# Optimization experiments

Hardware: AMD Instinct MI355X
Metric: run time of the kernel (lower is better)

Reference implementation:

```python
import jax, jax.numpy as jnp
import numpy as np

B, P, N, E, F, L = 64, 512, 512, 128, 512, 6
SQRT_E = 11.313708498984761
CLIP = 10.0
EPS = 1e-5

def _inorm(x, w, b):
    # InstanceNorm1d over node dim (axis=1) per (batch, channel); x: [B,N,E]
    mu = x.mean(axis=1, keepdims=True)
    var = x.var(axis=1, keepdims=True)
    return (x - mu) * jax.lax.rsqrt(var + EPS) * w + b

def setup_inputs():
    key = jax.random.key(0)
    ks = jax.random.split(key, 24)
    nrm = lambda k, shp, s=0.05: jax.random.normal(k, shp, dtype=jnp.float32) * s
    inp = {}
    inp['data'] = jax.random.uniform(ks[0], (B, N, 2), dtype=jnp.float32)
    inp['dist'] = -jax.random.uniform(ks[1], (B, N, N), dtype=jnp.float32)      # negative dist
    inp['cur_dist'] = -jax.random.uniform(ks[2], (B, P, N), dtype=jnp.float32)
    inp['capacity'] = jax.random.uniform(ks[3], (B, P), dtype=jnp.float32)
    inp['ninf_mask'] = jnp.zeros((B, P, N), jnp.float32)
    inp['log_scale'] = jnp.array([1.0], jnp.float32)
    # encoder params (Linear weights stored [in,out], i.e. torch weight transposed)
    inp['emb_W'] = nrm(ks[4], (2, E), 0.5); inp['emb_b'] = jnp.zeros((E,), jnp.float32)
    inp['Wq'] = nrm(ks[5], (L, E, E)); inp['Wk'] = nrm(ks[6], (L, E, E)); inp['Wv'] = nrm(ks[7], (L, E, E))
    inp['aft_alpha'] = jnp.ones((L,), jnp.float32)
    inp['n1_w'] = jnp.ones((L, E), jnp.float32); inp['n1_b'] = jnp.zeros((L, E), jnp.float32)
    inp['ff_W1'] = nrm(ks[8], (L, E, F)); inp['ff_b1'] = jnp.zeros((L, F), jnp.float32)
    inp['ff_W2'] = nrm(ks[9], (L, F, E)); inp['ff_b2'] = jnp.zeros((L, E), jnp.float32)
    inp['n2_w'] = jnp.ones((L, E), jnp.float32); inp['n2_b'] = jnp.zeros((L, E), jnp.float32)
    # decoder params
    inp['dWq'] = nrm(ks[10], (E + 1, E)); inp['dWk'] = nrm(ks[11], (E, E)); inp['dWv'] = nrm(ks[12], (E, E))
    inp['dec_aft_alpha'] = jnp.array([1.0], jnp.float32)
    inp['probs_alpha'] = jnp.array([1.0], jnp.float32)
    return inp

def reference(data, dist, cur_dist, capacity, ninf_mask, log_scale,
              emb_W, emb_b, Wq, Wk, Wv, aft_alpha, n1_w, n1_b,
              ff_W1, ff_b1, ff_W2, ff_b2, n2_w, n2_b,
              dWq, dWk, dWv, dec_aft_alpha, probs_alpha):
    ls = log_scale[0]
    # ---- encoder: stacked AFT layers ----
    x = data @ emb_W + emb_b                                   # [B,N,E]
    for l in range(L):
        q = x @ Wq[l]; k = x @ Wk[l]; v = x @ Wv[l]
        ad = jnp.exp(ls * aft_alpha[l] * dist)                 # [B,N,N]
        ek = jnp.exp(k)
        weighted = (ad @ (ek * v)) / (ad @ ek)                 # [B,N,E]
        out = jax.nn.sigmoid(q) * weighted
        h = _inorm(x + out, n1_w[l], n1_b[l])
        ff = jax.nn.relu(h @ ff_W1[l] + ff_b1[l]) @ ff_W2[l] + ff_b2[l]
        x = _inorm(h + ff, n2_w[l], n2_b[l])
    enc = x                                                    # [B,N,E]
    # ---- decoder ----
    k = enc @ dWk; v = enc @ dWv
    gmean = enc.mean(axis=1, keepdims=True)                    # [B,1,E]
    gmp = jnp.broadcast_to(gmean, (enc.shape[0], capacity.shape[1], enc.shape[2]))
    q = jnp.concatenate([gmp, capacity[:, :, None]], axis=2) @ dWq   # [B,P,E]
    ad = jnp.exp(ls * dec_aft_alpha[0] * cur_dist + ninf_mask)       # [B,P,N]
    ek = jnp.exp(k)
    weighted = (ad @ (ek * v)) / (ad @ ek)                     # [B,P,E]
    aft = jax.nn.sigmoid(q) * weighted
    score = jnp.einsum('bpe,bne->bpn', aft, enc) / SQRT_E
    score = score + ls * probs_alpha[0] * cur_dist
    score = CLIP * jnp.tanh(score) + ninf_mask
    return jax.nn.softmax(score, axis=2)                       # [B,P,N]
```

## Files before the change

### kernel.cpp

```cpp
#include <hip/hip_runtime.h>
#include <math.h>

#define B_ 64
#define N_ 512
#define P_ 512
#define E_ 128
#define F_ 512
#define L_ 6
#define SQRT_E_INV 0.08838834764831843f

typedef unsigned short u16;
typedef __attribute__((ext_vector_type(8))) short bf8;
typedef __attribute__((ext_vector_type(16))) float f16v;

__device__ inline u16 bf16r(float f) {
    unsigned u = __float_as_uint(f);
    u += 0x7fffu + ((u >> 16) & 1u);
    return (u16)(u >> 16);
}
__device__ inline float bf2f(u16 h) { return __uint_as_float((unsigned)h << 16); }

#define MFMA(a, b, c) __builtin_amdgcn_mfma_f32_32x32x16_bf16(a, b, c, 0, 0, 0)

struct QQ {
    const u16 *A0, *A1, *B0, *B1;
    u16* sq16;
};

__launch_bounds__(256, 4) __global__ void qvk_q_k(QQ p)
{
    const int tid = threadIdx.x;
    const int lane = tid & 63, wv = tid >> 6;
    const int wm = wv & 1, wn = wv >> 1;
    const int ln = lane & 31, hk = lane >> 5;
    const int row0 = blockIdx.x * 64;

    __shared__ __align__(16) u16 As[2][64][40];
    __shared__ __align__(16) u16 Bs[2][128][40];

    f16v acc[2];
#pragma unroll
    for (int nt = 0; nt < 2; ++nt)
#pragma unroll
        for (int q = 0; q < 16; ++q) acc[nt][q] = 0.f;

    const int r = tid >> 2, kq = tid & 3;
    for (int k0 = 0; k0 < 128; k0 += 32) {
        size_t ga = (size_t)(row0 + r) * 128 + k0 + kq * 8;
        *(uint4*)&As[0][r][kq * 8] = *(const uint4*)(p.A0 + ga);
        *(uint4*)&As[1][r][kq * 8] = *(const uint4*)(p.A1 + ga);
#pragma unroll
        for (int i = 0; i < 2; ++i) {
            int s = tid + i * 256;
            int rb = s >> 2, q = s & 3;
            size_t gb = (size_t)rb * 128 + k0 + q * 8;
            *(uint4*)&Bs[0][rb][q * 8] = *(const uint4*)(p.B0 + gb);
            *(uint4*)&Bs[1][rb][q * 8] = *(const uint4*)(p.B1 + gb);
        }
        __syncthreads();
#pragma unroll
        for (int s = 0; s < 2; ++s) {
            bf8 ah = *(const bf8*)&As[0][wm * 32 + ln][s * 16 + hk * 8];
            bf8 al = *(const bf8*)&As[1][wm * 32 + ln][s * 16 + hk * 8];
#pragma unroll
            for (int nt = 0; nt < 2; ++nt) {
                bf8 bh = *(const bf8*)&Bs[0][wn * 64 + nt * 32 + ln][s * 16 + hk * 8];
                bf8 bl = *(const bf8*)&Bs[1][wn * 64 + nt * 32 + ln][s * 16 + hk * 8];
                acc[nt] = MFMA(ah, bh, acc[nt]);
                acc[nt] = MFMA(ah, bl, acc[nt]);
                acc[nt] = MFMA(al, bh, acc[nt]);
            }
        }
        __syncthreads();
    }

#pragma unroll
    for (int nt = 0; nt < 2; ++nt) {
        int gn = wn * 64 + nt * 32 + ln;
#pragma unroll
        for (int g = 0; g < 4; ++g) {
            int rb = row0 + wm * 32 + g * 8 + hk * 4;
#pragma unroll
            for (int rr = 0; rr < 4; ++rr) {
                float v = acc[nt][g * 4 + rr];
                v = 1.f / (1.f + __expf(-v));
                p.sq16[(size_t)(rb + rr) * 128 + gn] = bf16r(v);
            }
        }
    }
}

struct QV {
    const u16 *A0, *A1;
    const u16 *vh, *vl, *kh, *kl;
    u16* y2t;
};

__launch_bounds__(256, 3) __global__ void qvk_vk_k(QV p)
{
    const int tid = threadIdx.x;
    const int lane = tid & 63, wv = tid >> 6;
    const int wm = wv & 1, wn = wv >> 1;
    const int ln = lane & 31, hk = lane >> 5;
    const int row0 = blockIdx.x * 64;

    __shared__ __align__(16) u16 As[2][64][40];
    __shared__ __align__(16) u16 Bs[4][128][40];

    f16v av[2], ak[2];
#pragma unroll
    for (int nt = 0; nt < 2; ++nt)
#pragma unroll
        for (int q = 0; q < 16; ++q) { av[nt][q] = 0.f; ak[nt][q] = 0.f; }

    const int r = tid >> 2, kq = tid & 3;
    for (int k0 = 0; k0 < 128; k0 += 32) {
        size_t ga = (size_t)(row0 + r) * 128 + k0 + kq * 8;
        *(uint4*)&As[0][r][kq * 8] = *(const uint4*)(p.A0 + ga);
        *(uint4*)&As[1][r][kq * 8] = *(const uint4*)(p.A1 + ga);
#pragma unroll
        for (int pl = 0; pl < 4; ++pl) {
            const u16* src = (pl == 0) ? p.vh : (pl == 1) ? p.vl
                             : (pl == 2) ? p.kh : p.kl;
#pragma unroll
            for (int i = 0; i < 2; ++i) {
                int s = tid + i * 256;
                int rb = s >> 2, q = s & 3;
                *(uint4*)&Bs[pl][rb][q * 8] =
                    *(const uint4*)(src + (size_t)rb * 128 + k0 + q * 8);
            }
        }
        __syncthreads();
#pragma unroll
        for (int s = 0; s < 2; ++s) {
            bf8 ah = *(const bf8*)&As[0][wm * 32 + ln][s * 16 + hk * 8];
            bf8 al = *(const bf8*)&As[1][wm * 32 + ln][s * 16 + hk * 8];
#pragma unroll
            for (int nt = 0; nt < 2; ++nt) {
                const int br = wn * 64 + nt * 32 + ln, sc = s * 16 + hk * 8;
                bf8 bvh = *(const bf8*)&Bs[0][br][sc];
                bf8 bvl = *(const bf8*)&Bs[1][br][sc];
                bf8 bkh = *(const bf8*)&Bs[2][br][sc];
                bf8 bkl = *(const bf8*)&Bs[3][br][sc];
                av[nt] = MFMA(ah, bvh, av[nt]);
                av[nt] = MFMA(ah, bvl, av[nt]);
                av[nt] = MFMA(al, bvh, av[nt]);
                ak[nt] = MFMA(ah, bkh, ak[nt]);
                ak[nt] = MFMA(ah, bkl, ak[nt]);
                ak[nt] = MFMA(al, bkh, ak[nt]);
            }
        }
        __syncthreads();
    }

#pragma unroll
    for (int nt = 0; nt < 2; ++nt) {
        int gn = wn * 64 + nt * 32 + ln;
#pragma unroll
        for (int g = 0; g < 4; ++g) {
            int rb = row0 + wm * 32 + g * 8 + hk * 4;
            int bb = rb >> 9, nb = rb & 511;
            u16 pe[4], pv[4];
#pragma unroll
            for (int rr = 0; rr < 4; ++rr) {
                u16 hv = bf16r(av[nt][g * 4 + rr]);
                u16 he = bf16r(__expf(ak[nt][g * 4 + rr]));
                pe[rr] = he;
                pv[rr] = bf16r(bf2f(hv) * bf2f(he));
            }
            uint2 ue, uv;
            ue.x = pe[0] | ((unsigned)pe[1] << 16);
            ue.y = pe[2] | ((unsigned)pe[3] << 16);
            uv.x = pv[0] | ((unsigned)pv[1] << 16);
            uv.y = pv[2] | ((unsigned)pv[3] << 16);
            *(uint2*)(p.y2t + (size_t)bb * 131072 + (size_t)gn * 512 + nb) = uv;
            *(uint2*)(p.y2t + (size_t)bb * 131072 + (size_t)(128 + gn) * 512 + nb) = ue;
        }
    }
}

struct AP2 {
    const float *A0, *A1;
    const u16 *B0, *sq;
    u16 *gh, *gl;
    const float *s1, *s2; int s2i;
};

template <int OPA, int SG>
__launch_bounds__(256, 2) __global__ void aft2_k(AP2 p)
{
    const int tid = threadIdx.x;
    const int lane = tid & 63, wv = tid >> 6;
    const int wm = wv & 1, wn = wv >> 1;
    const int ln = lane & 31, hk = lane >> 5;

    const int id = blockIdx.x;
    const int xcd = id & 7, slot = id >> 3;
    const int bz = xcd * 8 + (slot >> 3);
    const int row0 = (slot & 7) * 64;

    __shared__ __align__(16) u16 As[2][64][40];
    __shared__ __align__(16) u16 Bs[2][256][40];

    f16v acc[4];
#pragma unroll
    for (int j = 0; j < 4; ++j)
#pragma unroll
        for (int q = 0; q < 16; ++q) acc[j][q] = 0.f;

    const float ascale = p.s1[0] * p.s2[p.s2i];
    const float* Af = p.A0 + (size_t)bz * 262144 + (size_t)row0 * 512;
    const float* Mf = (OPA == 2)
        ? (p.A1 + (size_t)bz * 262144 + (size_t)row0 * 512) : (const float*)0;
    const u16* Bb = p.B0 + (size_t)bz * 131072;

    const int r = tid >> 2, kq = tid & 3;
    float fa[8], fm[8];
    uint4 vb[4];

#define AFT_LOAD(K0)                                                          \
    {                                                                         \
        size_t ga = (size_t)r * 512 + (K0) + kq * 8;                          \
// ... 48 lines not shown
        AFT_WRITE(cur ^ 1);
        __syncthreads();
        cur ^= 1;
    }
    AFT_COMPUTE(cur);

#undef AFT_LOAD
#undef AFT_WRITE
#undef AFT_COMPUTE

    const u16* sqb = SG ? (p.sq + (size_t)bz * 65536) : (const u16*)0;
    u16* ghb = p.gh + (size_t)bz * 65536;
    u16* glb = p.gl + (size_t)bz * 65536;
#pragma unroll
    for (int j = 0; j < 2; ++j) {
        int e = wn * 64 + j * 32 + ln;
#pragma unroll
        for (int g = 0; g < 4; ++g) {
#pragma unroll
            for (int rr = 0; rr < 4; ++rr) {
                int row = row0 + wm * 32 + g * 8 + hk * 4 + rr;
                float num = acc[j][g * 4 + rr];
                float den = acc[j + 2][g * 4 + rr];
                float pv = num / den;
                if (SG) pv *= bf2f(sqb[(size_t)row * 128 + e]);
                u16 hi = bf16r(pv);
                ghb[(size_t)row * 128 + e] = hi;
                glb[(size_t)row * 128 + e] = bf16r(pv - bf2f(hi));
            }
        }
    }
}

struct FP {
    const u16 *A0, *A1;
    const u16 *B0, *B1;
    const float* bias;
    u16* o16; float* of;
};

template <int PH>
__launch_bounds__(256, 4) __global__ void ffn_k(FP p)
{
    constexpr int AS = (PH == 1) ? 2 : 1;
    constexpr int K = (PH == 1) ? 128 : 512;
    const int tid = threadIdx.x;
    const int lane = tid & 63, wv = tid >> 6;
    const int wm = wv & 1, wn = wv >> 1;
    const int ln = lane & 31, hk = lane >> 5;
    int row0, colB0;
    if (PH == 1) {
        const int id = blockIdx.x;
        const int w = (id & 7) * 256 + (id >> 3);
        colB0 = (w & 3) * 128;
        row0 = (w >> 2) * 64;
    } else {
        row0 = blockIdx.x * 64;
        colB0 = 0;
    }

    __shared__ __align__(16) u16 As[AS][64][40];
    __shared__ __align__(16) u16 Bs[2][128][40];

    f16v acc[2];
#pragma unroll
    for (int nt = 0; nt < 2; ++nt)
#pragma unroll
        for (int q = 0; q < 16; ++q) acc[nt][q] = 0.f;

    const int r = tid >> 2, kq = tid & 3;
    for (int k0 = 0; k0 < K; k0 += 32) {
        size_t ga = (size_t)(row0 + r) * K + k0 + kq * 8;
        *(uint4*)&As[0][r][kq * 8] = *(const uint4*)(p.A0 + ga);
        if (AS == 2) *(uint4*)&As[1][r][kq * 8] = *(const uint4*)(p.A1 + ga);
#pragma unroll
        for (int i = 0; i < 2; ++i) {
            int s = tid + i * 256;
            int rb = s >> 2, q = s & 3;
            size_t gb = (size_t)(colB0 + rb) * K + k0 + q * 8;
            *(uint4*)&Bs[0][rb][q * 8] = *(const uint4*)(p.B0 + gb);
            *(uint4*)&Bs[1][rb][q * 8] = *(const uint4*)(p.B1 + gb);
        }
        __syncthreads();
#pragma unroll
        for (int s = 0; s < 2; ++s) {
            bf8 ah = *(const bf8*)&As[0][wm * 32 + ln][s * 16 + hk * 8];
            bf8 al;
            if (AS == 2) al = *(const bf8*)&As[1][wm * 32 + ln][s * 16 + hk * 8];
#pragma unroll
            for (int nt = 0; nt < 2; ++nt) {
                bf8 bh = *(const bf8*)&Bs[0][wn * 64 + nt * 32 + ln][s * 16 + hk * 8];
                bf8 bl = *(const bf8*)&Bs[1][wn * 64 + nt * 32 + ln][s * 16 + hk * 8];
                acc[nt] = MFMA(ah, bh, acc[nt]);
                acc[nt] = MFMA(ah, bl, acc[nt]);
                if (AS == 2) acc[nt] = MFMA(al, bh, acc[nt]);
            }
        }
        __syncthreads();
    }

#pragma unroll
    for (int nt = 0; nt < 2; ++nt) {
        int gcol = colB0 + wn * 64 + nt * 32 + ln;
        float bv = p.bias[gcol];
#pragma unroll
        for (int g = 0; g < 4; ++g) {
            int rb = row0 + wm * 32 + g * 8 + hk * 4;
#pragma unroll
            for (int rr = 0; rr < 4; ++rr) {
                float v = acc[nt][g * 4 + rr] + bv;
                if (PH == 1) {
                    v = fmaxf(v, 0.f);
                    p.o16[(size_t)(rb + rr) * 512 + gcol] = bf16r(v);
                } else {
                    p.of[(size_t)(rb + rr) * 128 + gcol] = v;
                }
            }
        }
    }
}

struct SP {
    const u16 *A0, *A1, *B0, *B1;
    float* Cf;
    const float *cd, *cm;
    const float *s1, *s2;
};

__launch_bounds__(256, 4) __global__ void score_k(SP p)
{
    const int tid = threadIdx.x;
    const int lane = tid & 63, wv = tid >> 6;
    const int wm = wv & 1, wn = wv >> 1;
    const int ln = lane & 31, hk = lane >> 5;

    const int id = blockIdx.x;
    const int xcd = id & 7, slot = id >> 3;
    const int bz = xcd * 8 + (slot >> 5);
    const int inner = slot & 31;
    const int row0 = (inner >> 2) * 64;
    const int colB0 = (inner & 3) * 128;

    __shared__ __align__(16) u16 As[2][64][40];
    __shared__ __align__(16) u16 Bs[2][128][40];

    f16v acc[2];
#pragma unroll
    for (int nt = 0; nt < 2; ++nt)
#pragma unroll
        for (int q = 0; q < 16; ++q) acc[nt][q] = 0.f;

    const int r = tid >> 2, kq = tid & 3;
    for (int k0 = 0; k0 < 128; k0 += 32) {
        size_t ga = (size_t)bz * 65536 + (size_t)(row0 + r) * 128 + k0 + kq * 8;
        *(uint4*)&As[0][r][kq * 8] = *(const uint4*)(p.A0 + ga);
        *(uint4*)&As[1][r][kq * 8] = *(const uint4*)(p.A1 + ga);
#pragma unroll
        for (int i = 0; i < 2; ++i) {
            int s = tid + i * 256;
            int rb = s >> 2, q = s & 3;
            size_t gb = (size_t)bz * 65536 + (size_t)(colB0 + rb) * 128 + k0 + q * 8;
            *(uint4*)&Bs[0][rb][q * 8] = *(const uint4*)(p.B0 + gb);
            *(uint4*)&Bs[1][rb][q * 8] = *(const uint4*)(p.B1 + gb);
        }
        __syncthreads();
#pragma unroll
        for (int s = 0; s < 2; ++s) {
            bf8 ah = *(const bf8*)&As[0][wm * 32 + ln][s * 16 + hk * 8];
            bf8 al = *(const bf8*)&As[1][wm * 32 + ln][s * 16 + hk * 8];
#pragma unroll
            for (int nt = 0; nt < 2; ++nt) {
                bf8 bh = *(const bf8*)&Bs[0][wn * 64 + nt * 32 + ln][s * 16 + hk * 8];
                bf8 bl = *(const bf8*)&Bs[1][wn * 64 + nt * 32 + ln][s * 16 + hk * 8];
                acc[nt] = MFMA(ah, bh, acc[nt]);
                acc[nt] = MFMA(ah, bl, acc[nt]);
                acc[nt] = MFMA(al, bh, acc[nt]);
            }
        }
        __syncthreads();
    }

    const float sp = p.s1[0] * p.s2[0];
#pragma unroll
    for (int nt = 0; nt < 2; ++nt) {
        int gn = colB0 + wn * 64 + nt * 32 + ln;
#pragma unroll
        for (int g = 0; g < 4; ++g) {
            int rb = row0 + wm * 32 + g * 8 + hk * 4;
#pragma unroll
            for (int rr = 0; rr < 4; ++rr) {
                float v = acc[nt][g * 4 + rr];
                size_t ix = (size_t)bz * 262144 + (size_t)(rb + rr) * 512 + gn;
                float sc = fmaf(v, SQRT_E_INV, sp * p.cd[ix]);
                float e2 = __expf(2.f * sc);
                float th = 1.f - 2.f / (e2 + 1.f);
                p.Cf[ix] = 10.f * th + p.cm[ix];
            }
        }
    }
}

template <int MODE>
__launch_bounds__(256) __global__ void inorm_k(
    const u16* __restrict__ ah, const u16* __restrict__ al,
    const u16* __restrict__ g0, const u16* __restrict__ g1,
    const float* __restrict__ f1,
    const float* __restrict__ nw, const float* __restrict__ nbv,
    u16* __restrict__ oh, u16* __restrict__ ol)
{
    const int bb = blockIdx.x, e0 = blockIdx.y * 16;
    const int tid = threadIdx.x, el = tid & 3, no = tid >> 2;
    const size_t base = (size_t)bb * N_ * E_ + e0 + el * 4;

    float4 vals[8];
    float s1x = 0, s1y = 0, s1z = 0, s1w = 0;
    float s2x = 0, s2y = 0, s2z = 0, s2w = 0;
#pragma unroll
    for (int i = 0; i < 8; ++i) {
        int n = no * 8 + i;
        size_t ad = base + (size_t)n * E_;
        uint2 h2 = *(const uint2*)(ah + ad);
        uint2 l2 = *(const uint2*)(al + ad);
        float x0 = bf2f((u16)h2.x) + bf2f((u16)l2.x);
        float x1 = bf2f((u16)(h2.x >> 16)) + bf2f((u16)(l2.x >> 16));
        float x2 = bf2f((u16)h2.y) + bf2f((u16)l2.y);
        float x3 = bf2f((u16)(h2.y >> 16)) + bf2f((u16)(l2.y >> 16));
        float4 v;
        if (MODE == 1) {
            uint2 a2 = *(const uint2*)(g0 + ad);
            uint2 b2 = *(const uint2*)(g1 + ad);
            v.x = x0 + bf2f((u16)a2.x) + bf2f((u16)b2.x);
            v.y = x1 + bf2f((u16)(a2.x >> 16)) + bf2f((u16)(b2.x >> 16));
            v.z = x2 + bf2f((u16)a2.y) + bf2f((u16)b2.y);
            v.w = x3 + bf2f((u16)(a2.y >> 16)) + bf2f((u16)(b2.y >> 16));
        } else {
            float4 ff = *(const float4*)(f1 + ad);
            v.x = x0 + ff.x; v.y = x1 + ff.y; v.z = x2 + ff.z; v.w = x3 + ff.w;
        }
        vals[i] = v;
        s1x += v.x; s1y += v.y; s1z += v.z; s1w += v.w;
        s2x = fmaf(v.x, v.x, s2x); s2y = fmaf(v.y, v.y, s2y);
        s2z = fmaf(v.z, v.z, s2z); s2w = fmaf(v.w, v.w, s2w);
    }

    __shared__ float4 r1[256], r2[256];
    r1[tid] = make_float4(s1x, s1y, s1z, s1w);
    r2[tid] = make_float4(s2x, s2y, s2z, s2w);
    __syncthreads();
    for (int s = 128; s >= 4; s >>= 1) {
        if (tid < s) {
            float4 u = r1[tid], w = r1[tid + s];
            r1[tid] = make_float4(u.x + w.x, u.y + w.y, u.z + w.z, u.w + w.w);
            float4 pq = r2[tid], q = r2[tid + s];
            r2[tid] = make_float4(pq.x + q.x, pq.y + q.y, pq.z + q.z, pq.w + q.w);
        }
        __syncthreads();
    }
    __shared__ float4 mu_s[4], rs_s[4];
    if (tid < 4) {
        float4 m = r1[tid], q = r2[tid];
        m.x *= (1.f / N_); m.y *= (1.f / N_); m.z *= (1.f / N_); m.w *= (1.f / N_);
        q.x *= (1.f / N_); q.y *= (1.f / N_); q.z *= (1.f / N_); q.w *= (1.f / N_);
        float4 rs;
        rs.x = rsqrtf(q.x - m.x * m.x + 1e-5f);
        rs.y = rsqrtf(q.y - m.y * m.y + 1e-5f);
        rs.z = rsqrtf(q.z - m.z * m.z + 1e-5f);
        rs.w = rsqrtf(q.w - m.w * m.w + 1e-5f);
        mu_s[tid] = m; rs_s[tid] = rs;
    }
    __syncthreads();
    float4 mu = mu_s[el], rs = rs_s[el];
    float4 w4 = *(const float4*)(nw + e0 + el * 4);
    float4 b4 = *(const float4*)(nbv + e0 + el * 4);
#pragma unroll
    for (int i = 0; i < 8; ++i) {
        size_t ad = base + (size_t)(no * 8 + i) * E_;
        float4 v = vals[i];
        v.x = fmaf((v.x - mu.x) * rs.x, w4.x, b4.x);
        v.y = fmaf((v.y - mu.y) * rs.y, w4.y, b4.y);
        v.z = fmaf((v.z - mu.z) * rs.z, w4.z, b4.z);
        v.w = fmaf((v.w - mu.w) * rs.w, w4.w, b4.w);
        u16 h0 = bf16r(v.x), h1 = bf16r(v.y), h2v = bf16r(v.z), h3 = bf16r(v.w);
        u16 l0 = bf16r(v.x - bf2f(h0)), l1 = bf16r(v.y - bf2f(h1));
        u16 l2v = bf16r(v.z - bf2f(h2v)), l3 = bf16r(v.w - bf2f(h3));
        uint2 ph, pl;
        ph.x = h0 | ((unsigned)h1 << 16); ph.y = h2v | ((unsigned)h3 << 16);
        pl.x = l0 | ((unsigned)l1 << 16); pl.y = l2v | ((unsigned)l3 << 16);
        *(uint2*)(oh + ad) = ph;
        *(uint2*)(ol + ad) = pl;
    }
}

__global__ void wprep_k(const float* __restrict__ W, u16* __restrict__ Th,
                        u16* __restrict__ Tl, int K, int N)
{
    const int z = blockIdx.z;
    const float* Wz = W + (size_t)z * K * N;
    u16* Hh = Th + (size_t)z * K * N;
    u16* Hl = Tl + (size_t)z * K * N;
    __shared__ float t[32][33];
    const int j = threadIdx.x & 31, i0 = threadIdx.x >> 5;
    const int k0 = blockIdx.x * 32, n0 = blockIdx.y * 32;
    for (int i = i0; i < 32; i += 8)
        t[i][j] = Wz[(size_t)(k0 + i) * N + n0 + j];
    __syncthreads();
    for (int i = i0; i < 32; i += 8) {
        float v = t[j][i];
        u16 h = bf16r(v);
        u16 l = bf16r(v - bf2f(h));
        size_t o = (size_t)(n0 + i) * K + k0 + j;
        Hh[o] = h; Hl[o] = l;
    }
}

// ... 22 lines not shown
        size_t ix = ((size_t)b * N_ + n) * E_ + e;
        s += bf2f(xh[ix]) + bf2f(xl[ix]);
    }
    __shared__ float part[512];
    __shared__ float gm[128];
    part[tid] = s;
    __syncthreads();
    if (tid < 128)
        gm[tid] = (part[tid] + part[tid + 128] + part[tid + 256] + part[tid + 384]) *
                  (1.f / N_);
    __syncthreads();
    if (tid < 128) {
        float acc = 0.f;
        for (int kk = 0; kk < 128; ++kk) acc = fmaf(gm[kk], dWq[kk * 128 + tid], acc);
        gq[b * 128 + tid] = acc;
    }
}

__global__ void dec_aft_k(const float* __restrict__ gq, const float* __restrict__ cap,
                          const float* __restrict__ dWq,
                          const u16* __restrict__ rh, const u16* __restrict__ rl,
                          u16* __restrict__ oh, u16* __restrict__ ol)
{
    size_t idx = (size_t)blockIdx.x * 256 + threadIdx.x;
    int e = idx & 127;
    size_t bp = idx >> 7;
    int b = (int)(bp >> 9);
    float q = fmaf(cap[bp], dWq[128 * 128 + e], gq[b * 128 + e]);
    float sg = 1.f / (1.f + __expf(-q));
    float v = sg * (bf2f(rh[idx]) + bf2f(rl[idx]));
    u16 h = bf16r(v);
    oh[idx] = h;
    ol[idx] = bf16r(v - bf2f(h));
}

__launch_bounds__(256) __global__ void softmax_k(float* __restrict__ out)
{
    int row = blockIdx.x * 4 + (threadIdx.x >> 6);
    int lane = threadIdx.x & 63;
    float* p = out + (size_t)row * 512 + lane * 8;
    float4 v0 = *(float4*)p;
    float4 v1 = *(float4*)(p + 4);
    float m = fmaxf(fmaxf(fmaxf(v0.x, v0.y), fmaxf(v0.z, v0.w)),
                    fmaxf(fmaxf(v1.x, v1.y), fmaxf(v1.z, v1.w)));
#pragma unroll
    for (int o = 32; o; o >>= 1) m = fmaxf(m, __shfl_xor(m, o));
    v0.x = __expf(v0.x - m); v0.y = __expf(v0.y - m);
    v0.z = __expf(v0.z - m); v0.w = __expf(v0.w - m);
    v1.x = __expf(v1.x - m); v1.y = __expf(v1.y - m);
    v1.z = __expf(v1.z - m); v1.w = __expf(v1.w - m);
    float s = v0.x + v0.y + v0.z + v0.w + v1.x + v1.y + v1.z + v1.w;
#pragma unroll
    for (int o = 32; o; o >>= 1) s += __shfl_xor(s, o);
    float inv = 1.f / s;
    v0.x *= inv; v0.y *= inv; v0.z *= inv; v0.w *= inv;
    v1.x *= inv; v1.y *= inv; v1.z *= inv; v1.w *= inv;
    *(float4*)p = v0;
    *(float4*)(p + 4) = v1;
}

extern "C" void kernel_launch(void* const* d_in, const int* in_sizes, int n_in,
                              void* d_out, int out_size, void* d_ws, size_t ws_size,
                              hipStream_t stream)
{
    const float* data      = (const float*)d_in[0];
    const float* dist      = (const float*)d_in[1];
    const float* cur_dist  = (const float*)d_in[2];
    const float* capacity  = (const float*)d_in[3];
    const float* ninf      = (const float*)d_in[4];
    const float* log_scale = (const float*)d_in[5];
    const float* emb_W     = (const float*)d_in[6];
    const float* emb_b     = (const float*)d_in[7];
    const float* Wq        = (const float*)d_in[8];
    const float* Wk        = (const float*)d_in[9];
    const float* Wv        = (const float*)d_in[10];
    const float* aft_alpha = (const float*)d_in[11];
    const float* n1_w      = (const float*)d_in[12];
    const float* n1_b      = (const float*)d_in[13];
    const float* ffW1      = (const float*)d_in[14];
    const float* ffb1      = (const float*)d_in[15];
    const float* ffW2      = (const float*)d_in[16];
    const float* ffb2      = (const float*)d_in[17];
    const float* n2_w      = (const float*)d_in[18];
    const float* n2_b      = (const float*)d_in[19];
    const float* dWq       = (const float*)d_in[20];
    const float* dWk       = (const float*)d_in[21];
    const float* dWv       = (const float*)d_in[22];
    const float* dec_alpha = (const float*)d_in[23];
    const float* p_alpha   = (const float*)d_in[24];
    float* out = (float*)d_out;

    char* W = (char*)d_ws;
    size_t off = 0;
    auto take = [&](size_t n) { void* pp = W + off; off += (n + 255) & ~(size_t)255; return pp; };
    const size_t SZP = (size_t)B_ * N_ * E_ * 2;

    u16* xh   = (u16*)take(SZP);
    u16* xl   = (u16*)take(SZP);
    u16* hh   = (u16*)take(SZP);
    u16* hl   = (u16*)take(SZP);
    u16* sq16 = (u16*)take(SZP);
    u16* gh   = (u16*)take(SZP);
    u16* gl   = (u16*)take(SZP);
    u16* y2t  = (u16*)take(2 * SZP);
    float* ff2 = (float*)take((size_t)B_ * N_ * E_ * 4);
    u16* wqt_h = (u16*)take(196608); u16* wqt_l = (u16*)take(196608);
    u16* wkt_h = (u16*)take(196608); u16* wkt_l = (u16*)take(196608);
    u16* wvt_h = (u16*)take(196608); u16* wvt_l = (u16*)take(196608);
    u16* w1t_h = (u16*)take(786432); u16* w1t_l = (u16*)take(786432);
    u16* w2t_h = (u16*)take(786432); u16* w2t_l = (u16*)take(786432);
    u16* dkt_h = (u16*)take(32768);  u16* dkt_l = (u16*)take(32768);
    u16* dvt_h = (u16*)take(32768);  u16* dvt_l = (u16*)take(32768);
    float* gq = (float*)take(32768);
    if (ws_size < off) return;

    u16* ff1 = sq16;

    wprep_k<<<dim3(4, 4, 6), 256, 0, stream>>>(Wq, wqt_h, wqt_l, 128, 128);
    wprep_k<<<dim3(4, 4, 6), 256, 0, stream>>>(Wk, wkt_h, wkt_l, 128, 128);
    wprep_k<<<dim3(4, 4, 6), 256, 0, stream>>>(Wv, wvt_h, wvt_l, 128, 128);
    wprep_k<<<dim3(4, 16, 6), 256, 0, stream>>>(ffW1, w1t_h, w1t_l, 128, 512);
    wprep_k<<<dim3(16, 4, 6), 256, 0, stream>>>(ffW2, w2t_h, w2t_l, 512, 128);
    wprep_k<<<dim3(4, 4, 1), 256, 0, stream>>>(dWk, dkt_h, dkt_l, 128, 128);
    wprep_k<<<dim3(4, 4, 1), 256, 0, stream>>>(dWv, dvt_h, dvt_l, 128, 128);

    embed_k<<<16384, 256, 0, stream>>>(data, emb_W, emb_b, xh, xl);

    for (int l = 0; l < L_; ++l) {
        QQ qq{};
        qq.A0 = xh; qq.A1 = xl;
        qq.B0 = wqt_h + l * 16384; qq.B1 = wqt_l + l * 16384;
        qq.sq16 = sq16;
        qvk_q_k<<<512, 256, 0, stream>>>(qq);

        QV qv{};
        qv.A0 = xh; qv.A1 = xl;
        qv.vh = wvt_h + l * 16384; qv.vl = wvt_l + l * 16384;
        qv.kh = wkt_h + l * 16384; qv.kl = wkt_l + l * 16384;
        qv.y2t = y2t;
        qvk_vk_k<<<512, 256, 0, stream>>>(qv);

        AP2 ap{};
        ap.A0 = dist; ap.B0 = y2t; ap.sq = sq16; ap.gh = gh; ap.gl = gl;
        ap.s1 = log_scale; ap.s2 = aft_alpha; ap.s2i = l;
        aft2_k<1, 1><<<512, 256, 0, stream>>>(ap);

        inorm_k<1><<<dim3(B_, 8), 256, 0, stream>>>(
            xh, xl, gh, gl, nullptr, n1_w + l * 128, n1_b + l * 128, hh, hl);

        FP fp{};
        fp.A0 = hh; fp.A1 = hl;
        fp.B0 = w1t_h + l * 65536; fp.B1 = w1t_l + l * 65536;
        fp.bias = ffb1 + l * 512; fp.o16 = ff1;
        ffn_k<1><<<2048, 256, 0, stream>>>(fp);

        fp = FP{};
        fp.A0 = ff1;
        fp.B0 = w2t_h + l * 65536; fp.B1 = w2t_l + l * 65536;
        fp.bias = ffb2 + l * 128; fp.of = ff2;
        ffn_k<2><<<dim3(512, 1), 256, 0, stream>>>(fp);

        inorm_k<2><<<dim3(B_, 8), 256, 0, stream>>>(
            hh, hl, nullptr, nullptr, ff2, n2_w + l * 128, n2_b + l * 128, xh, xl);
    }

    {
        QV qv{};
        qv.A0 = xh; qv.A1 = xl;
        qv.vh = dvt_h; qv.vl = dvt_l;
        qv.kh = dkt_h; qv.kl = dkt_l;
        qv.y2t = y2t;
        qvk_vk_k<<<512, 256, 0, stream>>>(qv);
        gq_k<<<B_, 512, 0, stream>>>(xh, xl, dWq, gq);

        AP2 ap{};
        ap.A0 = cur_dist; ap.A1 = ninf; ap.B0 = y2t; ap.gh = gh; ap.gl = gl;
        ap.s1 = log_scale; ap.s2 = dec_alpha; ap.s2i = 0;
        aft2_k<2, 0><<<512, 256, 0, stream>>>(ap);

        dec_aft_k<<<16384, 256, 0, stream>>>(gq, capacity, dWq, gh, gl, hh, hl);

        SP sp{};
        sp.A0 = hh; sp.A1 = hl; sp.B0 = xh; sp.B1 = xl;
        sp.Cf = out; sp.cd = cur_dist; sp.cm = ninf;
        sp.s1 = log_scale; sp.s2 = p_alpha;
        score_k<<<2048, 256, 0, stream>>>(sp);

        softmax_k<<<8192, 256, 0, stream>>>(out);
    }
}
```

Before: 1.170 ms.

## Fuse QKV projections, FFN up/down, and decoder score with softmax

New measurement: 1.198 ms. +2.4%, slower.

```diff
diff --git a/kernel.cpp b/kernel.cpp
--- a/kernel.cpp
+++ b/kernel.cpp
@@ -22,12 +22,13 @@
 
 #define MFMA(a, b, c) __builtin_amdgcn_mfma_f32_32x32x16_bf16(a, b, c, 0, 0, 0)
 
-struct QQ {
-    const u16 *A0, *A1, *B0, *B1;
-    u16* sq16;
+struct Q3 {
+    const u16 *A0, *A1;
+    const u16 *qh, *ql, *vh, *vl, *kh, *kl;
+    u16 *sq16, *y2t;
 };
 
-__launch_bounds__(256, 4) __global__ void qvk_q_k(QQ p)
+__launch_bounds__(256, 2) __global__ void qvk3_k(Q3 p)
 {
     const int tid = threadIdx.x;
     const int lane = tid & 63, wv = tid >> 6;
@@ -36,13 +37,13 @@
     const int row0 = blockIdx.x * 64;
 
     __shared__ __align__(16) u16 As[2][64][40];
-    __shared__ __align__(16) u16 Bs[2][128][40];
-
-    f16v acc[2];
+    __shared__ __align__(16) u16 Bs[6][128][40];
+
+    f16v aq[2], av[2], ak[2];
 #pragma unroll
     for (int nt = 0; nt < 2; ++nt)
 #pragma unroll
-        for (int q = 0; q < 16; ++q) acc[nt][q] = 0.f;
+        for (int q = 0; q < 16; ++q) { aq[nt][q] = 0.f; av[nt][q] = 0.f; ak[nt][q] = 0.f; }
 
     const int r = tid >> 2, kq = tid & 3;
     for (int k0 = 0; k0 < 128; k0 += 32) {
@@ -52,10 +53,14 @@
 #pragma unroll
         for (int i = 0; i < 2; ++i) {
             int s = tid + i * 256;
-            int rb = s >> 2, q = s & 3;
-            size_t gb = (size_t)rb * 128 + k0 + q * 8;
-            *(uint4*)&Bs[0][rb][q * 8] = *(const uint4*)(p.B0 + gb);
-            *(uint4*)&Bs[1][rb][q * 8] = *(const uint4*)(p.B1 + gb);
+            int rb2 = s >> 2, q = s & 3;
+            size_t gb = (size_t)rb2 * 128 + k0 + q * 8;
+            *(uint4*)&Bs[0][rb2][q * 8] = *(const uint4*)(p.qh + gb);
+            *(uint4*)&Bs[1][rb2][q * 8] = *(const uint4*)(p.ql + gb);
+            *(uint4*)&Bs[2][rb2][q * 8] = *(const uint4*)(p.vh + gb);
+            *(uint4*)&Bs[3][rb2][q * 8] = *(const uint4*)(p.vl + gb);
+            *(uint4*)&Bs[4][rb2][q * 8] = *(const uint4*)(p.kh + gb);
+            *(uint4*)&Bs[5][rb2][q * 8] = *(const uint4*)(p.kl + gb);
         }
         __syncthreads();
 #pragma unroll
@@ -64,11 +69,22 @@
             bf8 al = *(const bf8*)&As[1][wm * 32 + ln][s * 16 + hk * 8];
 #pragma unroll
             for (int nt = 0; nt < 2; ++nt) {
-                bf8 bh = *(const bf8*)&Bs[0][wn * 64 + nt * 32 + ln][s * 16 + hk * 8];
-                bf8 bl = *(const bf8*)&Bs[1][wn * 64 + nt * 32 + ln][s * 16 + hk * 8];
-                acc[nt] = MFMA(ah, bh, acc[nt]);
-                acc[nt] = MFMA(ah, bl, acc[nt]);
-                acc[nt] = MFMA(al, bh, acc[nt]);
+                const int br = wn * 64 + nt * 32 + ln, sc = s * 16 + hk * 8;
+                bf8 bqh = *(const bf8*)&Bs[0][br][sc];
+                bf8 bql = *(const bf8*)&Bs[1][br][sc];
+                bf8 bvh = *(const bf8*)&Bs[2][br][sc];
+                bf8 bvl = *(const bf8*)&Bs[3][br][sc];
+                bf8 bkh = *(const bf8*)&Bs[4][br][sc];
+                bf8 bkl = *(const bf8*)&Bs[5][br][sc];
+                aq[nt] = MFMA(ah, bqh, aq[nt]);
+                aq[nt] = MFMA(ah, bql, aq[nt]);
+                aq[nt] = MFMA(al, bqh, aq[nt]);
+                av[nt] = MFMA(ah, bvh, av[nt]);
+                av[nt] = MFMA(ah, bvl, av[nt]);
+                av[nt] = MFMA(al, bvh, av[nt]);
+                ak[nt] = MFMA(ah, bkh, ak[nt]);
+                ak[nt] = MFMA(ah, bkl, ak[nt]);
+                ak[nt] = MFMA(al, bkh, ak[nt]);
             }
         }
         __syncthreads();
@@ -80,12 +96,25 @@
 #pragma unroll
         for (int g = 0; g < 4; ++g) {
             int rb = row0 + wm * 32 + g * 8 + hk * 4;
+            int bb = rb >> 9, nb = rb & 511;
+            u16 pe[4], pv[4];
 #pragma unroll
             for (int rr = 0; rr < 4; ++rr) {
-                float v = acc[nt][g * 4 + rr];
-                v = 1.f / (1.f + __expf(-v));
-                p.sq16[(size_t)(rb + rr) * 128 + gn] = bf16r(v);
+                float vq = aq[nt][g * 4 + rr];
+                p.sq16[(size_t)(rb + rr) * 128 + gn] =
+                    bf16r(1.f / (1.f + __expf(-vq)));
+                u16 hv = bf16r(av[nt][g * 4 + rr]);
+                u16 he = bf16r(__expf(ak[nt][g * 4 + rr]));
+                pe[rr] = he;
+                pv[rr] = bf16r(bf2f(hv) * bf2f(he));
             }
+            uint2 ue, uv;
+            ue.x = pe[0] | ((unsigned)pe[1] << 16);
+            ue.y = pe[2] | ((unsigned)pe[3] << 16);
+            uv.x = pv[0] | ((unsigned)pv[1] << 16);
+            uv.y = pv[2] | ((unsigned)pv[3] << 16);
+            *(uint2*)(p.y2t + (size_t)bb * 131072 + (size_t)gn * 512 + nb) = uv;
+            *(uint2*)(p.y2t + (size_t)bb * 131072 + (size_t)(128 + gn) * 512 + nb) = ue;
         }
     }
 }
@@ -119,16 +148,14 @@
         *(uint4*)&As[0][r][kq * 8] = *(const uint4*)(p.A0 + ga);
         *(uint4*)&As[1][r][kq * 8] = *(const uint4*)(p.A1 + ga);
 #pragma unroll
-        for (int pl = 0; pl < 4; ++pl) {
-            const u16* src = (pl == 0) ? p.vh : (pl == 1) ? p.vl
-                             : (pl == 2) ? p.kh : p.kl;
-#pragma unroll
-            for (int i = 0; i < 2; ++i) {
-                int s = tid + i * 256;
-                int rb = s >> 2, q = s & 3;
-                *(uint4*)&Bs[pl][rb][q * 8] =
-                    *(const uint4*)(src + (size_t)rb * 128 + k0 + q * 8);
-            }
+        for (int i = 0; i < 2; ++i) {
+            int s = tid + i * 256;
+            int rb2 = s >> 2, q = s & 3;
+            size_t gb = (size_t)rb2 * 128 + k0 + q * 8;
+            *(uint4*)&Bs[0][rb2][q * 8] = *(const uint4*)(p.vh + gb);
+            *(uint4*)&Bs[1][rb2][q * 8] = *(const uint4*)(p.vl + gb);
+            *(uint4*)&Bs[2][rb2][q * 8] = *(const uint4*)(p.kh + gb);
+            *(uint4*)&Bs[3][rb2][q * 8] = *(const uint4*)(p.kl + gb);
         }
         __syncthreads();
 #pragma unroll
@@ -187,7 +214,7 @@
 };
 
 template <int OPA, int SG>
-__launch_bounds__(256, 2) __global__ void aft2_k(AP2 p)
+__launch_bounds__(256, 3) __global__ void aft2_k(AP2 p)
 {
     const int tid = threadIdx.x;
     const int lane = tid & 63, wv = tid >> 6;
@@ -302,102 +329,117 @@
     }
 }
 
-struct FP {
+struct F12 {
     const u16 *A0, *A1;
-    const u16 *B0, *B1;
-    const float* bias;
-    u16* o16; float* of;
+    const u16 *w1h, *w1l;
+    const u16 *w2h, *w2l;
+    const float *b1, *b2;
+    float* of;
 };
 
-template <int PH>
-__launch_bounds__(256, 4) __global__ void ffn_k(FP p)
-{
-    constexpr int AS = (PH == 1) ? 2 : 1;
-    constexpr int K = (PH == 1) ? 128 : 512;
+__launch_bounds__(512, 2) __global__ void ffn12_k(F12 p)
+{
     const int tid = threadIdx.x;
     const int lane = tid & 63, wv = tid >> 6;
     const int wm = wv & 1, wn = wv >> 1;
     const int ln = lane & 31, hk = lane >> 5;
-    int row0, colB0;
-    if (PH == 1) {
-        const int id = blockIdx.x;
-        const int w = (id & 7) * 256 + (id >> 3);
-        colB0 = (w & 3) * 128;
-        row0 = (w >> 2) * 64;
-    } else {
-        row0 = blockIdx.x * 64;
-        colB0 = 0;
-    }
-
-    __shared__ __align__(16) u16 As[AS][64][40];
-    __shared__ __align__(16) u16 Bs[2][128][40];
-
-    f16v acc[2];
-#pragma unroll
-    for (int nt = 0; nt < 2; ++nt)
-#pragma unroll
-        for (int q = 0; q < 16; ++q) acc[nt][q] = 0.f;
-
-    const int r = tid >> 2, kq = tid & 3;
-    for (int k0 = 0; k0 < K; k0 += 32) {
-        size_t ga = (size_t)(row0 + r) * K + k0 + kq * 8;
-        *(uint4*)&As[0][r][kq * 8] = *(const uint4*)(p.A0 + ga);
-        if (AS == 2) *(uint4*)&As[1][r][kq * 8] = *(const uint4*)(p.A1 + ga);
-#pragma unroll
-        for (int i = 0; i < 2; ++i) {
-            int s = tid + i * 256;
-            int rb = s >> 2, q = s & 3;
-            size_t gb = (size_t)(colB0 + rb) * K + k0 + q * 8;
-            *(uint4*)&Bs[0][rb][q * 8] = *(const uint4*)(p.B0 + gb);
-            *(uint4*)&Bs[1][rb][q * 8] = *(const uint4*)(p.B1 + gb);
-        }
-        __syncthreads();
-#pragma unroll
-        for (int s = 0; s < 2; ++s) {
-            bf8 ah = *(const bf8*)&As[0][wm * 32 + ln][s * 16 + hk * 8];
-            bf8 al;
-            if (AS == 2) al = *(const bf8*)&As[1][wm * 32 + ln][s * 16 + hk * 8];
-#pragma unroll
-            for (int nt = 0; nt < 2; ++nt) {
-                bf8 bh = *(const bf8*)&Bs[0][wn * 64 + nt * 32 + ln][s * 16 + hk * 8];
-                bf8 bl = *(const bf8*)&Bs[1][wn * 64 + nt * 32 + ln][s * 16 + hk * 8];
-                acc[nt] = MFMA(ah, bh, acc[nt]);
-                acc[nt] = MFMA(ah, bl, acc[nt]);
-                if (AS == 2) acc[nt] = MFMA(al, bh, acc[nt]);
+    const int row0 = blockIdx.x * 64;
+
+    __shared__ __align__(16) u16 Bs[2][128][136];
+    __shared__ __align__(16) u16 ff1c[4][64][136];
+
+    bf8 ar0[8], ar1[8];
+    {
+        const size_t arow = (size_t)(row0 + wm * 32 + ln) * 128;
+#pragma unroll
+        for (int s = 0; s < 8; ++s) {
+            ar0[s] = *(const bf8*)(p.A0 + arow + s * 16 + hk * 8);
+            ar1[s] = *(const bf8*)(p.A1 + arow + s * 16 + hk * 8);
+        }
+    }
+
+    const int lcol = wn * 32 + ln;
+
+    for (int ct = 0; ct < 4; ++ct) {
+#pragma unroll
+        for (int i = 0; i < 4; ++i) {
+            int idx = tid + i * 512;
+            int col = idx >> 4, q = idx & 15;
+            size_t gb = (size_t)(ct * 128 + col) * 128 + q * 8;
+            *(uint4*)&Bs[0][col][q * 8] = *(const uint4*)(p.w1h + gb);
+            *(uint4*)&Bs[1][col][q * 8] = *(const uint4*)(p.w1l + gb);
+        }
+        __syncthreads();
+
+        f16v a0, a1, a2;
+#pragma unroll
+        for (int q = 0; q < 16; ++q) { a0[q] = 0.f; a1[q] = 0.f; a2[q] = 0.f; }
+#pragma unroll
+        for (int s = 0; s < 8; ++s) {
+            bf8 bh = *(const bf8*)&Bs[0][lcol][s * 16 + hk * 8];
+            bf8 bl = *(const bf8*)&Bs[1][lcol][s * 16 + hk * 8];
+            a0 = MFMA(ar0[s], bh, a0);
+            a1 = MFMA(ar0[s], bl, a1);
+            a2 = MFMA(ar1[s], bh, a2);
+        }
+        __syncthreads();
+
+        float bv = p.b1[ct * 128 + lcol];
+#pragma unroll
+        for (int g = 0; g < 4; ++g) {
+#pragma unroll
+            for (int rr = 0; rr < 4; ++rr) {
+                int lr = wm * 32 + g * 8 + hk * 4 + rr;
+                float v = a0[g * 4 + rr] + a1[g * 4 + rr] + a2[g * 4 + rr] + bv;
+                ff1c[ct][lr][lcol] = bf16r(fmaxf(v, 0.f));
             }
         }
-        __syncthreads();
-    }
-
-#pragma unroll
-    for (int nt = 0; nt < 2; ++nt) {
-        int gcol = colB0 + wn * 64 + nt * 32 + ln;
-        float bv = p.bias[gcol];
-#pragma unroll
-        for (int g = 0; g < 4; ++g) {
-            int rb = row0 + wm * 32 + g * 8 + hk * 4;
-#pragma unroll
-            for (int rr = 0; rr < 4; ++rr) {
-                float v = acc[nt][g * 4 + rr] + bv;
-                if (PH == 1) {
-                    v = fmaxf(v, 0.f);
-                    p.o16[(size_t)(rb + rr) * 512 + gcol] = bf16r(v);
-                } else {
-                    p.of[(size_t)(rb + rr) * 128 + gcol] = v;
-                }
-            }
-        }
-    }
-}
-
-struct SP {
+    }
+    __syncthreads();
+
+    f16v c0, c1;
+#pragma unroll
+    for (int q = 0; q < 16; ++q) { c0[q] = 0.f; c1[q] = 0.f; }
+    for (int kc = 0; kc < 4; ++kc) {
+#pragma unroll
+        for (int i = 0; i < 4; ++i) {
+            int idx = tid + i * 512;
+            int col = idx >> 4, q = idx & 15;
+            size_t gb = (size_t)col * 512 + kc * 128 + q * 8;
+            *(uint4*)&Bs[0][col][q * 8] = *(const uint4*)(p.w2h + gb);
+            *(uint4*)&Bs[1][col][q * 8] = *(const uint4*)(p.w2l + gb);
+        }
+        __syncthreads();
+#pragma unroll
+        for (int s = 0; s < 8; ++s) {
+            bf8 af = *(const bf8*)&ff1c[kc][wm * 32 + ln][s * 16 + hk * 8];
+            bf8 bh = *(const bf8*)&Bs[0][lcol][s * 16 + hk * 8];
+            bf8 bl = *(const bf8*)&Bs[1][lcol][s * 16 + hk * 8];
+            c0 = MFMA(af, bh, c0);
+            c1 = MFMA(af, bl, c1);
+        }
+        __syncthreads();
+    }
+
+    float bv = p.b2[lcol];
+#pragma unroll
+    for (int g = 0; g < 4; ++g) {
+#pragma unroll
+        for (int rr = 0; rr < 4; ++rr) {
+            int rb = row0 + wm * 32 + g * 8 + hk * 4 + rr;
+            p.of[(size_t)rb * 128 + lcol] = c0[g * 4 + rr] + c1[g * 4 + rr] + bv;
+        }
+    }
+}
+
+struct SP2 {
     const u16 *A0, *A1, *B0, *B1;
-    float* Cf;
+    float* out;
     const float *cd, *cm;
     const float *s1, *s2;
 };
 
-__launch_bounds__(256, 4) __global__ void score_k(SP p)
+__launch_bounds__(256, 2) __global__ void score_sm_k(SP2 p)
 {
     const int tid = threadIdx.x;
     const int lane = tid & 63, wv = tid >> 6;
@@ -405,69 +447,121 @@
     const int ln = lane & 31, hk = lane >> 5;
 
     const int id = blockIdx.x;
-    const int xcd = id & 7, slot = id >> 3;
-    const int bz = xcd * 8 + (slot >> 5);
-    const int inner = slot & 31;
-    const int row0 = (inner >> 2) * 64;
-    const int colB0 = (inner & 3) * 128;
-
-    __shared__ __align__(16) u16 As[2][64][40];
-    __shared__ __align__(16) u16 Bs[2][128][40];
-
-    f16v acc[2];
-#pragma unroll
-    for (int nt = 0; nt < 2; ++nt)
-#pragma unroll
-        for (int q = 0; q < 16; ++q) acc[nt][q] = 0.f;
-
-    const int r = tid >> 2, kq = tid & 3;
-    for (int k0 = 0; k0 < 128; k0 += 32) {
-        size_t ga = (size_t)bz * 65536 + (size_t)(row0 + r) * 128 + k0 + kq * 8;
-        *(uint4*)&As[0][r][kq * 8] = *(const uint4*)(p.A0 + ga);
-        *(uint4*)&As[1][r][kq * 8] = *(const uint4*)(p.A1 + ga);
-#pragma unroll
-        for (int i = 0; i < 2; ++i) {
-            int s = tid + i * 256;
-            int rb = s >> 2, q = s & 3;
-            size_t gb = (size_t)bz * 65536 + (size_t)(colB0 + rb) * 128 + k0 + q * 8;
-            *(uint4*)&Bs[0][rb][q * 8] = *(const uint4*)(p.B0 + gb);
-            *(uint4*)&Bs[1][rb][q * 8] = *(const uint4*)(p.B1 + gb);
-        }
-        __syncthreads();
-#pragma unroll
-        for (int s = 0; s < 2; ++s) {
-            bf8 ah = *(const bf8*)&As[0][wm * 32 + ln][s * 16 + hk * 8];
-            bf8 al = *(const bf8*)&As[1][wm * 32 + ln][s * 16 + hk * 8];
-#pragma unroll
-            for (int nt = 0; nt < 2; ++nt) {
-                bf8 bh = *(const bf8*)&Bs[0][wn * 64 + nt * 32 + ln][s * 16 + hk * 8];
-                bf8 bl = *(const bf8*)&Bs[1][wn * 64 + nt * 32 + ln][s * 16 + hk * 8];
-                acc[nt] = MFMA(ah, bh, acc[nt]);
-                acc[nt] = MFMA(ah, bl, acc[nt]);
-                acc[nt] = MFMA(al, bh, acc[nt]);
+    const int xcd = id & 7, s_ = id >> 3;
+    const int bz = xcd * 8 + (s_ & 7);
+    const int row0 = (s_ >> 3) * 64;
+
+    __shared__ __align__(16) u16 As[2][64][136];
+    __shared__ __align__(16) u16 Bs[2][128][72];
+    __shared__ float rs[2][64];
+
+#pragma unroll
+    for (int i = 0; i < 8; ++i) {
+        int idx = tid + i * 256;
+        int pl = idx >> 10, rem = idx & 1023;
+        int row = rem >> 4, q = rem & 15;
+        const u16* src = pl ? p.A1 : p.A0;
+        *(uint4*)&As[pl][row][q * 8] =
+            *(const uint4*)(src + ((size_t)bz * 512 + row0 + row) * 128 + q * 8);
+    }
+
+    const float sp = p.s1[0] * p.s2[0];
+    f16v accs[4][2];
+    float rsum[16];
+#pragma unroll
+    for (int i = 0; i < 16; ++i) rsum[i] = 0.f;
+
+#pragma unroll
+    for (int ct = 0; ct < 4; ++ct) {
+#pragma unroll
+        for (int nt = 0; nt < 2; ++nt)
+#pragma unroll
+            for (int q = 0; q < 16; ++q) accs[ct][nt][q] = 0.f;
+
+        for (int kc = 0; kc < 128; kc += 64) {
+#pragma unroll
+            for (int i = 0; i < 8; ++i) {
+                int idx = tid + i * 256;
+                int pl = idx >> 10, rem = idx & 1023;
+                int row = rem >> 3, q = rem & 7;
+                const u16* src = pl ? p.B1 : p.B0;
+                *(uint4*)&Bs[pl][row][q * 8] =
+                    *(const uint4*)(src + ((size_t)bz * 512 + ct * 128 + row) * 128
+                                    + kc + q * 8);
             }
-        }
-        __syncthreads();
-    }
-
-    const float sp = p.s1[0] * p.s2[0];
-#pragma unroll
-    for (int nt = 0; nt < 2; ++nt) {
-        int gn = colB0 + wn * 64 + nt * 32 + ln;
-#pragma unroll
-        for (int g = 0; g < 4; ++g) {
-            int rb = row0 + wm * 32 + g * 8 + hk * 4;
-#pragma unroll
-            for (int rr = 0; rr < 4; ++rr) {
-                float v = acc[nt][g * 4 + rr];
-                size_t ix = (size_t)bz * 262144 + (size_t)(rb + rr) * 512 + gn;
-                float sc = fmaf(v, SQRT_E_INV, sp * p.cd[ix]);
-                float e2 = __expf(2.f * sc);
-                float th = 1.f - 2.f / (e2 + 1.f);
-                p.Cf[ix] = 10.f * th + p.cm[ix];
+            __syncthreads();
+#pragma unroll
+            for (int s = 0; s < 4; ++s) {
+                bf8 ah = *(const bf8*)&As[0][wm * 32 + ln][kc + s * 16 + hk * 8];
+                bf8 al = *(const bf8*)&As[1][wm * 32 + ln][kc + s * 16 + hk * 8];
+#pragma unroll
+                for (int nt = 0; nt < 2; ++nt) {
+                    bf8 bh = *(const bf8*)&Bs[0][wn * 64 + nt * 32 + ln][s * 16 + hk * 8];
+                    bf8 bl = *(const bf8*)&Bs[1][wn * 64 + nt * 32 + ln][s * 16 + hk * 8];
+                    accs[ct][nt] = MFMA(ah, bh, accs[ct][nt]);
+                    accs[ct][nt] = MFMA(ah, bl, accs[ct][nt]);
+                    accs[ct][nt] = MFMA(al, bh, accs[ct][nt]);
+                }
             }
-        }
-    }
+            __syncthreads();
+        }
+
+#pragma unroll
+        for (int nt = 0; nt < 2; ++nt) {
+            int gn = ct * 128 + wn * 64 + nt * 32 + ln;
+#pragma unroll
+            for (int g = 0; g < 4; ++g) {
+#pragma unroll
+                for (int rr = 0; rr < 4; ++rr) {
+                    int grow = row0 + wm * 32 + g * 8 + hk * 4 + rr;
+                    size_t ix = (size_t)bz * 262144 + (size_t)grow * 512 + gn;
+                    float sc = fmaf(accs[ct][nt][g * 4 + rr], SQRT_E_INV,
+                                    sp * p.cd[ix]);
+                    float e2 = __expf(2.f * sc);
+                    float th = 1.f - 2.f / (e2 + 1.f);
+                    float ev = __expf(10.f * th + p.cm[ix]);
+                    accs[ct][nt][g * 4 + rr] = ev;
+                    rsum[g * 4 + rr] += ev;
+                }
+            }
+        }
+    }
+
+#pragma unroll
+    for (int i = 0; i < 16; ++i) {
+#pragma unroll
+        for (int o = 1; o < 32; o <<= 1) rsum[i] += __shfl_xor(rsum[i], o);
+    }
+    __syncthreads();
+    if (ln == 0) {
+#pragma unroll
+        for (int i = 0; i < 16; ++i) {
+            int lr = wm * 32 + (i >> 2) * 8 + hk * 4 + (i & 3);
+            rs[wn][lr] = rsum[i];
+        }
+    }
+    __syncthreads();
+    float invr[16];
+#pragma unroll
+    for (int i = 0; i < 16; ++i) {
+        int lr = wm * 32 + (i >> 2) * 8 + hk * 4 + (i & 3);
+        invr[i] = 1.f / (rs[0][lr] + rs[1][lr]);
+    }
+
+#pragma unroll
+    for (int ct = 0; ct < 4; ++ct)
+#pragma unroll
+        for (int nt = 0; nt < 2; ++nt) {
+            int gn = ct * 128 + wn * 64 + nt * 32 + ln;
+#pragma unroll
+            for (int g = 0; g < 4; ++g)
+#pragma unroll
+                for (int rr = 0; rr < 4; ++rr) {
+                    int grow = row0 + wm * 32 + g * 8 + hk * 4 + rr;
+                    size_t ix = (size_t)bz * 262144 + (size_t)grow * 512 + gn;
+                    p.out[ix] = accs[ct][nt][g * 4 + rr] * invr[g * 4 + rr];
+                }
+        }
 }
 
 template <int MODE>
@@ -531,25 +625,25 @@
         float4 m = r1[tid], q = r2[tid];
         m.x *= (1.f / N_); m.y *= (1.f / N_); m.z *= (1.f / N_); m.w *= (1.f / N_);
         q.x *= (1.f / N_); q.y *= (1.f / N_); q.z *= (1.f / N_); q.w *= (1.f / N_);
-        float4 rs;
-        rs.x = rsqrtf(q.x - m.x * m.x + 1e-5f);
-        rs.y = rsqrtf(q.y - m.y * m.y + 1e-5f);
-        rs.z = rsqrtf(q.z - m.z * m.z + 1e-5f);
-        rs.w = rsqrtf(q.w - m.w * m.w + 1e-5f);
-        mu_s[tid] = m; rs_s[tid] = rs;
+        float4 rsq;
+        rsq.x = rsqrtf(q.x - m.x * m.x + 1e-5f);
+        rsq.y = rsqrtf(q.y - m.y * m.y + 1e-5f);
+        rsq.z = rsqrtf(q.z - m.z * m.z + 1e-5f);
+        rsq.w = rsqrtf(q.w - m.w * m.w + 1e-5f);
+        mu_s[tid] = m; rs_s[tid] = rsq;
     }
     __syncthreads();
-    float4 mu = mu_s[el], rs = rs_s[el];
+    float4 mu = mu_s[el], rsq = rs_s[el];
     float4 w4 = *(const float4*)(nw + e0 + el * 4);
     float4 b4 = *(const float4*)(nbv + e0 + el * 4);
 #pragma unroll
     for (int i = 0; i < 8; ++i) {
         size_t ad = base + (size_t)(no * 8 + i) * E_;
         float4 v = vals[i];
-        v.x = fmaf((v.x - mu.x) * rs.x, w4.x, b4.x);
-        v.y = fmaf((v.y - mu.y) * rs.y, w4.y, b4.y);
-        v.z = fmaf((v.z - mu.z) * rs.z, w4.z, b4.z);
-        v.w = fmaf((v.w - mu.w) * rs.w, w4.w, b4.w);
+        v.x = fmaf((v.x - mu.x) * rsq.x, w4.x, b4.x);
+        v.y = fmaf((v.y - mu.y) * rsq.y, w4.y, b4.y);
+        v.z = fmaf((v.z - mu.z) * rsq.z, w4.z, b4.z);
+        v.w = fmaf((v.w - mu.w) * rsq.w, w4.w, b4.w);
         u16 h0 = bf16r(v.x), h1 = bf16r(v.y), h2v = bf16r(v.z), h3 = bf16r(v.w);
         u16 l0 = bf16r(v.x - bf2f(h0)), l1 = bf16r(v.y - bf2f(h1));
         u16 l2v = bf16r(v.z - bf2f(h2v)), l3 = bf16r(v.w - bf2f(h3));
@@ -638,31 +732,6 @@
     u16 h = bf16r(v);
     oh[idx] = h;
     ol[idx] = bf16r(v - bf2f(h));
-}
-
-__launch_bounds__(256) __global__ void softmax_k(float* __restrict__ out)
-{
-    int row = blockIdx.x * 4 + (threadIdx.x >> 6);
-    int lane = threadIdx.x & 63;
-    float* p = out + (size_t)row * 512 + lane * 8;
-    float4 v0 = *(float4*)p;
-    float4 v1 = *(float4*)(p + 4);
-    float m = fmaxf(fmaxf(fmaxf(v0.x, v0.y), fmaxf(v0.z, v0.w)),
-                    fmaxf(fmaxf(v1.x, v1.y), fmaxf(v1.z, v1.w)));
-#pragma unroll
-    for (int o = 32; o; o >>= 1) m = fmaxf(m, __shfl_xor(m, o));
-    v0.x = __expf(v0.x - m); v0.y = __expf(v0.y - m);
-    v0.z = __expf(v0.z - m); v0.w = __expf(v0.w - m);
-    v1.x = __expf(v1.x - m); v1.y = __expf(v1.y - m);
-    v1.z = __expf(v1.z - m); v1.w = __expf(v1.w - m);
-    float s = v0.x + v0.y + v0.z + v0.w + v1.x + v1.y + v1.z + v1.w;
-#pragma unroll
-    for (int o = 32; o; o >>= 1) s += __shfl_xor(s, o);
-    float inv = 1.f / s;
-    v0.x *= inv; v0.y *= inv; v0.z *= inv; v0.w *= inv;
-    v1.x *= inv; v1.y *= inv; v1.z *= inv; v1.w *= inv;
-    *(float4*)p = v0;
-    *(float4*)(p + 4) = v1;
 }
 
 extern "C" void kernel_launch(void* const* d_in, const int* in_sizes, int n_in,
@@ -720,8 +789,6 @@
     float* gq = (float*)take(32768);
     if (ws_size < off) return;
 
-    u16* ff1 = sq16;
-
     wprep_k<<<dim3(4, 4, 6), 256, 0, stream>>>(Wq, wqt_h, wqt_l, 128, 128);
     wprep_k<<<dim3(4, 4, 6), 256, 0, stream>>>(Wk, wkt_h, wkt_l, 128, 128);
     wprep_k<<<dim3(4, 4, 6), 256, 0, stream>>>(Wv, wvt_h, wvt_l, 128, 128);
@@ -733,18 +800,13 @@
     embed_k<<<16384, 256, 0, stream>>>(data, emb_W, emb_b, xh, xl);
 
     for (int l = 0; l < L_; ++l) {
-        QQ qq{};
-        qq.A0 = xh; qq.A1 = xl;
-        qq.B0 = wqt_h + l * 16384; qq.B1 = wqt_l + l * 16384;
-        qq.sq16 = sq16;
-        qvk_q_k<<<512, 256, 0, stream>>>(qq);
-
-        QV qv{};
-        qv.A0 = xh; qv.A1 = xl;
-        qv.vh = wvt_h + l * 16384; qv.vl = wvt_l + l * 16384;
-        qv.kh = wkt_h + l * 16384; qv.kl = wkt_l + l * 16384;
-        qv.y2t = y2t;
-        qvk_vk_k<<<512, 256, 0, stream>>>(qv);
+        Q3 q3{};
+        q3.A0 = xh; q3.A1 = xl;
+        q3.qh = wqt_h + l * 16384; q3.ql = wqt_l + l * 16384;
+        q3.vh = wvt_h + l * 16384; q3.vl = wvt_l + l * 16384;
+        q3.kh = wkt_h + l * 16384; q3.kl = wkt_l + l * 16384;
+        q3.sq16 = sq16; q3.y2t = y2t;
+        qvk3_k<<<512, 256, 0, stream>>>(q3);
 
         AP2 ap{};
         ap.A0 = dist; ap.B0 = y2t; ap.sq = sq16; ap.gh = gh; ap.gl = gl;
@@ -754,17 +816,13 @@
         inorm_k<1><<<dim3(B_, 8), 256, 0, stream>>>(
             xh, xl, gh, gl, nullptr, n1_w + l * 128, n1_b + l * 128, hh, hl);
 
-        FP fp{};
-        fp.A0 = hh; fp.A1 = hl;
-        fp.B0 = w1t_h + l * 65536; fp.B1 = w1t_l + l * 65536;
-        fp.bias = ffb1 + l * 512; fp.o16 = ff1;
-        ffn_k<1><<<2048, 256, 0, stream>>>(fp);
-
-        fp = FP{};
-        fp.A0 = ff1;
-        fp.B0 = w2t_h + l * 65536; fp.B1 = w2t_l + l * 65536;
-        fp.bias = ffb2 + l * 128; fp.of = ff2;
-        ffn_k<2><<<dim3(512, 1), 256, 0, stream>>>(fp);
+        F12 f12{};
+        f12.A0 = hh; f12.A1 = hl;
+        f12.w1h = w1t_h + l * 65536; f12.w1l = w1t_l + l * 65536;
+        f12.w2h = w2t_h + l * 65536; f12.w2l = w2t_l + l * 65536;
+        f12.b1 = ffb1 + l * 512; f12.b2 = ffb2 + l * 128;
+        f12.of = ff2;
+        ffn12_k<<<512, 512, 0, stream>>>(f12);
 
         inorm_k<2><<<dim3(B_, 8), 256, 0, stream>>>(
             hh, hl, nullptr, nullptr, ff2, n2_w + l * 128, n2_b + l * 128, xh, xl);
@@ -786,12 +844,10 @@
 
         dec_aft_k<<<16384, 256, 0, stream>>>(gq, capacity, dWq, gh, gl, hh, hl);
 
-        SP sp{};
+        SP2 sp{};
         sp.A0 = hh; sp.A1 = hl; sp.B0 = xh; sp.B1 = xl;
-        sp.Cf = out; sp.cd = cur_dist; sp.cm = ninf;
+        sp.out = out; sp.cd = cur_dist; sp.cm = ninf;
         sp.s1 = log_scale; sp.s2 = p_alpha;
-        score_k<<<2048, 256, 0, stream>>>(sp);
-
-        softmax_k<<<8192, 256, 0, stream>>>(out);
-    }
-}
+        score_sm_k<<<512, 256, 0, stream>>>(sp);
+    }
+}
```
